# Performance work log

Hardware: AMD Instinct MI355X
Metric: run time of the kernel (lower is better)

The kernel has to match this reference:

```python
import jax, jax.numpy as jnp
import numpy as np

N_NODES = 50000
N_EDGES = 800000
D_IN = 256
D_OUT = 256


def setup_inputs() -> dict:
    key = jax.random.key(0)
    ks = jax.random.split(key, 8)
    x = jax.random.normal(ks[0], (N_NODES, D_IN), dtype=jnp.float32)
    edge_index = jax.random.randint(ks[1], (2, N_EDGES), 0, N_NODES, dtype=jnp.int64)
    W_src = jax.random.normal(ks[2], (D_IN, D_OUT), dtype=jnp.float32) * 0.05
    b_src = jax.random.normal(ks[3], (D_OUT,), dtype=jnp.float32) * 0.05
    W_dst = jax.random.normal(ks[4], (D_IN, D_OUT), dtype=jnp.float32) * 0.05
    b_dst = jax.random.normal(ks[5], (D_OUT,), dtype=jnp.float32) * 0.05
    W_self = jax.random.normal(ks[6], (D_IN, D_OUT), dtype=jnp.float32) * 0.05
    b_self = jax.random.normal(ks[7], (D_OUT,), dtype=jnp.float32) * 0.05
    return {"x": x, "edge_index": edge_index, "W_src": W_src, "b_src": b_src,
            "W_dst": W_dst, "b_dst": b_dst, "W_self": W_self, "b_self": b_self}


def reference(x, edge_index, W_src, b_src, W_dst, b_dst, W_self, b_self):
    # LEConv: messages = src_linear(x[row]) - dst_linear(x[col]);
    # scatter-add messages into destination nodes (col); add self_linear(x).
    # Linear commutes with row-gather, so project once on [N, d] then gather.
    row, col = edge_index[0], edge_index[1]
    src = x @ W_src + b_src            # [N, D_OUT]
    dst = x @ W_dst + b_dst            # [N, D_OUT]
    messages = src[row] - dst[col]     # [E, D_OUT]
    agg = jax.ops.segment_sum(messages, col, num_segments=x.shape[0])  # [N, D_OUT]
    return x @ W_self + b_self + agg
```

## Files before the change

### kernel.cpp

```cpp
#include <hip/hip_runtime.h>

#define D 256

typedef unsigned short ushort_t;
typedef unsigned int uint_t;
typedef __attribute__((ext_vector_type(8))) short short8;
typedef __attribute__((ext_vector_type(4))) float floatx4;

static __device__ __forceinline__ ushort_t f2bf(float f) {
    union { float f; uint_t u; } c; c.f = f;
    uint_t r = (c.u + 0x7FFFu + ((c.u >> 16) & 1u)) >> 16;
    return (ushort_t)r;
}
static __device__ __forceinline__ float bf2f(ushort_t b) {
    union { uint_t u; float f; } c; c.u = ((uint_t)b) << 16;
    return c.f;
}

static __device__ __forceinline__ void async16(const void* g, void* l) {
    __builtin_amdgcn_global_load_lds(
        (const __attribute__((address_space(1))) void*)g,
        (__attribute__((address_space(3))) void*)l, 16, 0, 0);
}

__global__ void prep_kernel(const int* __restrict__ col, int* __restrict__ deg,
                            int* __restrict__ rank,
                            const float* __restrict__ x, ushort_t* __restrict__ xh,
                            const float* __restrict__ Wself, const float* __restrict__ Wsrc,
                            const float* __restrict__ Wdst, ushort_t* __restrict__ BT,
                            int E, int total8, int degB, int cvtB) {
    int b = blockIdx.x;
    if (b < degB) {
        int e = b * 256 + threadIdx.x;
        if (e < E) rank[e] = atomicAdd(&deg[col[e]], 1);
    } else if (b < degB + cvtB) {
        int i = (b - degB) * 256 + threadIdx.x;
        if (i >= total8) return;
        float4 a = ((const float4*)x)[i * 2];
        float4 bb = ((const float4*)x)[i * 2 + 1];
        uint4 o;
        o.x = f2bf(a.x) | ((uint_t)f2bf(a.y) << 16);
        o.y = f2bf(a.z) | ((uint_t)f2bf(a.w) << 16);
        o.z = f2bf(bb.x) | ((uint_t)f2bf(bb.y) << 16);
        o.w = f2bf(bb.z) | ((uint_t)f2bf(bb.w) << 16);
        ((uint4*)xh)[i] = o;
    } else {
        int id = (b - degB - cvtB) * 256 + threadIdx.x;
        if (id >= 256 * 768) return;
        int j = id / 768, k = id % 768;
        float v;
        if (k < 256)      v = Wself[(size_t)k * 256 + j];
        else if (k < 512) v = Wsrc [(size_t)(k - 256) * 256 + j];
        else              v = Wdst [(size_t)(k - 512) * 256 + j];
        BT[id] = f2bf(v);
    }
}

__global__ __launch_bounds__(256) void scanA(const int* __restrict__ deg,
                                             int* __restrict__ off,
                                             int* __restrict__ partials, int n4) {
    __shared__ int wtot[4];
    const int tid = threadIdx.x, lane = tid & 63, wid = tid >> 6;
    int i4 = blockIdx.x * 256 + tid;
    int4 v = (i4 < n4) ? ((const int4*)deg)[i4] : make_int4(0, 0, 0, 0);
    int s = v.x + v.y + v.z + v.w;
    int incl = s;
    #pragma unroll
    for (int st = 1; st < 64; st <<= 1) {
        int t = __shfl_up(incl, st, 64);
        if (lane >= st) incl += t;
    }
    if (lane == 63) wtot[wid] = incl;
    __syncthreads();
    int wbase = 0;
    #pragma unroll
    for (int w = 0; w < 4; ++w) if (w < wid) wbase += wtot[w];
    int excl = incl - s + wbase;
    if (i4 < n4) {
        int4 o;
        o.x = excl; o.y = o.x + v.x; o.z = o.y + v.y; o.w = o.z + v.z;
        ((int4*)off)[i4] = o;
    }
    if (tid == 0) partials[blockIdx.x] = wtot[0] + wtot[1] + wtot[2] + wtot[3];
}

__global__ __launch_bounds__(256) void scanC(int* __restrict__ off,
                                             const int* __restrict__ partials, int n4) {
    __shared__ int base_s;
    const int tid = threadIdx.x;
    if (tid < 64) {
        int v = (tid < blockIdx.x) ? partials[tid] : 0;
        #pragma unroll
        for (int st = 32; st; st >>= 1) v += __shfl_down(v, st, 64);
        if (tid == 0) base_s = v;
    }
    __syncthreads();
    int base = base_s;
    int i4 = blockIdx.x * 256 + tid;
    if (i4 < n4) {
        int4 o = ((int4*)off)[i4];
        o.x += base; o.y += base; o.z += base; o.w += base;
        ((int4*)off)[i4] = o;
    }
}

__global__ void fill_kernel(const int* __restrict__ row, const int* __restrict__ col,
                            const int* __restrict__ rank, const int* __restrict__ off,
                            int* __restrict__ bucket, int E) {
    int e = blockIdx.x * blockDim.x + threadIdx.x;
    if (e >= E) return;
    bucket[off[col[e]] + rank[e]] = row[e];
}

__global__ __launch_bounds__(256) void segsum_kernel(const ushort_t* __restrict__ xh,
                                                     const int* __restrict__ off,
                                                     const int* __restrict__ deg,
                                                     const int* __restrict__ bucket,
                                                     ushort_t* __restrict__ Gh, int N) {
    int node = blockIdx.x * 4 + (threadIdx.x >> 6);
    int lane = threadIdx.x & 63;
    if (node >= N) return;
    int start = off[node];
    int cnt = deg[node];
    float a0 = 0.f, a1 = 0.f, a2 = 0.f, a3 = 0.f;
    int i = 0;
    for (; i + 4 <= cnt; i += 4) {
        int r0 = bucket[start + i];
        int r1 = bucket[start + i + 1];
        int r2 = bucket[start + i + 2];
        int r3 = bucket[start + i + 3];
        ushort4 v0 = ((const ushort4*)(xh + (size_t)r0 * D))[lane];
        ushort4 v1 = ((const ushort4*)(xh + (size_t)r1 * D))[lane];
        ushort4 v2 = ((const ushort4*)(xh + (size_t)r2 * D))[lane];
        ushort4 v3 = ((const ushort4*)(xh + (size_t)r3 * D))[lane];
        a0 += (bf2f(v0.x) + bf2f(v1.x)) + (bf2f(v2.x) + bf2f(v3.x));
        a1 += (bf2f(v0.y) + bf2f(v1.y)) + (bf2f(v2.y) + bf2f(v3.y));
        a2 += (bf2f(v0.z) + bf2f(v1.z)) + (bf2f(v2.z) + bf2f(v3.z));
        a3 += (bf2f(v0.w) + bf2f(v1.w)) + (bf2f(v2.w) + bf2f(v3.w));
    }
    for (; i < cnt; ++i) {
        int r0 = bucket[start + i];
        ushort4 v0 = ((const ushort4*)(xh + (size_t)r0 * D))[lane];
        a0 += bf2f(v0.x); a1 += bf2f(v0.y); a2 += bf2f(v0.z); a3 += bf2f(v0.w);
    }
    ushort4 o;
    o.x = f2bf(a0); o.y = f2bf(a1); o.z = f2bf(a2); o.w = f2bf(a3);
    ((ushort4*)(Gh + (size_t)node * D))[lane] = o;
}

__global__ __launch_bounds__(256, 2) void mfma_gemm(
    const ushort_t* __restrict__ xh, const ushort_t* __restrict__ Gh,
    const ushort_t* __restrict__ BT, const int* __restrict__ deg,
    const float* __restrict__ bsrc, const float* __restrict__ bdst,
    const float* __restrict__ bself, float* __restrict__ out, int N)
{
    __shared__ ushort_t As[2][8][64][8];
    __shared__ ushort_t Bs[2][8][64][8];
    __shared__ ushort_t Ds[2][8][64][8];

    const int tid = threadIdx.x;
    const int lane = tid & 63, wave = tid >> 6;
    const int quad = lane >> 4, l15 = lane & 15;
    const int mg = (wave >> 1) * 4, ng = (wave & 1) * 4;
    const int mbase = blockIdx.x * 128, nbase = blockIdx.y * 128;

    const int ga0 = wave * 2, ga1 = ga0 + 1;
    int ar0 = mbase + ga0 * 16 + l15; if (ar0 >= N) ar0 = N - 1;
    int ar1 = mbase + ga1 * 16 + l15; if (ar1 >= N) ar1 = N - 1;
    const size_t aoff0 = (size_t)ar0 * 256 + quad * 8;
    const size_t aoff1 = (size_t)ar1 * 256 + quad * 8;
    const ushort_t* bp0 = BT + (size_t)(nbase + ga0 * 16 + l15) * 768 + quad * 8;
    const ushort_t* bp1 = BT + (size_t)(nbase + ga1 * 16 + l15) * 768 + quad * 8;

    floatx4 acc1[4][4] = {};
    floatx4 acc2[4][4] = {};

    async16(xh + aoff0, &As[0][ga0][0][0]);
    async16(xh + aoff1, &As[0][ga1][0][0]);
    async16(bp0, &Bs[0][ga0][0][0]);
    async16(bp1, &Bs[0][ga1][0][0]);
    async16(bp0 + 512, &Ds[0][ga0][0][0]);
    async16(bp1 + 512, &Ds[0][ga1][0][0]);
    asm volatile("s_waitcnt vmcnt(0)" ::: "memory");
    __builtin_amdgcn_s_barrier();

    #pragma unroll
    for (int kt = 0; kt < 16; ++kt) {
        const int cur = kt & 1, nxt = cur ^ 1;

        if (kt < 15) {
            const int k1 = kt + 1;
            const ushort_t* Asrc = (k1 < 8) ? xh : Gh;
            const int ka = (k1 & 7) * 32;
            const int kb = k1 * 32;
            async16(Asrc + aoff0 + ka, &As[nxt][ga0][0][0]);
            async16(Asrc + aoff1 + ka, &As[nxt][ga1][0][0]);
            async16(bp0 + kb, &Bs[nxt][ga0][0][0]);
            async16(bp1 + kb, &Bs[nxt][ga1][0][0]);
            if (k1 < 8) {
                async16(bp0 + 512 + kb, &Ds[nxt][ga0][0][0]);
                async16(bp1 + 512 + kb, &Ds[nxt][ga1][0][0]);
            }
        }

        short8 af[4], bfr[4];
        #pragma unroll
        for (int im = 0; im < 4; ++im)
            af[im] = *(const short8*)(&As[cur][mg + im][lane][0]);
        #pragma unroll
        for (int in = 0; in < 4; ++in)
            bfr[in] = *(const short8*)(&Bs[cur][ng + in][lane][0]);
        short8 df[4];
        if (kt < 8) {
            #pragma unroll
            for (int in = 0; in < 4; ++in)
                df[in] = *(const short8*)(&Ds[cur][ng + in][lane][0]);
        }
        asm volatile("s_waitcnt lgkmcnt(0)" ::: "memory");
        #pragma unroll
        for (int im = 0; im < 4; ++im)
            #pragma unroll
            for (int in = 0; in < 4; ++in)
                acc1[im][in] = __builtin_amdgcn_mfma_f32_16x16x32_bf16(
                    af[im], bfr[in], acc1[im][in], 0, 0, 0);
        if (kt < 8) {
            #pragma unroll
            for (int im = 0; im < 4; ++im)
                #pragma unroll
                for (int in = 0; in < 4; ++in)
                    acc2[im][in] = __builtin_amdgcn_mfma_f32_16x16x32_bf16(
                        af[im], df[in], acc2[im][in], 0, 0, 0);
        }

        if (kt < 15) {
            asm volatile("s_waitcnt vmcnt(0)" ::: "memory");
            __builtin_amdgcn_s_barrier();
        }
    }

    float degv[4][4];
    #pragma unroll
    for (int im = 0; im < 4; ++im)
        #pragma unroll
        for (int r = 0; r < 4; ++r) {
            int gm = mbase + (wave >> 1) * 64 + im * 16 + quad * 4 + r;
            degv[im][r] = (gm < N) ? (float)deg[gm] : 0.f;
        }

    #pragma unroll
    for (int in = 0; in < 4; ++in) {
        int gn = nbase + (wave & 1) * 64 + in * 16 + l15;
        float bs = bself[gn];
        float db = bsrc[gn] - bdst[gn];
        #pragma unroll
        for (int im = 0; im < 4; ++im) {
            #pragma unroll
            for (int r = 0; r < 4; ++r) {
                int gm = mbase + (wave >> 1) * 64 + im * 16 + quad * 4 + r;
                if (gm < N) {
                    float d = degv[im][r];
                    out[(size_t)gm * 256 + gn] =
                        acc1[im][in][r] - d * acc2[im][in][r] + bs + d * db;
                }
            }
        }
    }
}

extern "C" void kernel_launch(void* const* d_in, const int* in_sizes, int n_in,
                              void* d_out, int out_size, void* d_ws, size_t ws_size,
                              hipStream_t stream) {
    const float* x     = (const float*)d_in[0];
    const int*   eidx  = (const int*)d_in[1];
    const float* Wsrc  = (const float*)d_in[2];
    const float* bsrc  = (const float*)d_in[3];
    const float* Wdst  = (const float*)d_in[4];
    const float* bdst  = (const float*)d_in[5];
    const float* Wself = (const float*)d_in[6];
    const float* bself = (const float*)d_in[7];
    float* out = (float*)d_out;

    const int N = in_sizes[0] / D;
    const int E = in_sizes[1] / 2;
    const int* row = eidx;
    const int* col = eidx + E;

    char* p = (char*)d_ws;
    ushort_t* xh  = (ushort_t*)p;        p += (size_t)N * D * sizeof(ushort_t);
    ushort_t* Gh  = (ushort_t*)p;        int* rank = (int*)p;
                                         p += (size_t)N * D * sizeof(ushort_t);
    ushort_t* BT  = (ushort_t*)p;        p += (size_t)768 * 256 * sizeof(ushort_t);
    int* deg      = (int*)p;             p += (size_t)N * sizeof(int);
    int* off      = (int*)p;             p += (size_t)N * sizeof(int);
    int* partials = (int*)p;             p += 64 * sizeof(int);
    int* bucket   = (int*)p;

    hipMemsetAsync(deg, 0, (size_t)N * sizeof(int), stream);

    const int total8 = N * D / 8;
    const int degB = (E + 255) / 256;
    const int cvtB = (total8 + 255) / 256;
    const int btB  = (256 * 768 + 255) / 256;
    prep_kernel<<<degB + cvtB + btB, 256, 0, stream>>>(col, deg, rank, x, xh,
                                                       Wself, Wsrc, Wdst, BT,
                                                       E, total8, degB, cvtB);
    const int n4 = N / 4;
    const int nblk = (n4 + 255) / 256;
    scanA<<<nblk, 256, 0, stream>>>(deg, off, partials, n4);
    scanC<<<nblk, 256, 0, stream>>>(off, partials, n4);
    fill_kernel<<<(E + 255) / 256, 256, 0, stream>>>(row, col, rank, off, bucket, E);
    segsum_kernel<<<(N + 3) / 4, 256, 0, stream>>>(xh, off, deg, bucket, Gh, N);

    dim3 grid((N + 127) / 128, 2);
    mfma_gemm<<<grid, 256, 0, stream>>>(xh, Gh, BT, deg, bsrc, bdst, bself, out, N);
}
```

Measured before the change: 277.6 us.

## Fold degree-scaled dst term into A operand and shrink GEMM M-tile to 64

The dst-projection term is no longer kept in a separate accumulator. Instead it becomes a third K segment in which the x rows are pre-scaled by -deg in bf16 before the MFMA, giving a single K=768 GEMM with one accumulator set. The block M-tile drops from 128 to 64, the Ds LDS buffer is removed and launch bounds are raised to 4 blocks per CU, which lowers register and LDS pressure for higher occupancy. In exchange, per-element scaling work is added in the inner loop, B tiles are reused less, and rounding deg*x to bf16 can reduce accuracy.

```diff
diff --git a/kernel.cpp b/kernel.cpp
--- a/kernel.cpp
+++ b/kernel.cpp
@@ -148,119 +148,111 @@
     ((ushort4*)(Gh + (size_t)node * D))[lane] = o;
 }
 
-__global__ __launch_bounds__(256, 2) void mfma_gemm(
+__global__ __launch_bounds__(256, 4) void mfma_gemm(
     const ushort_t* __restrict__ xh, const ushort_t* __restrict__ Gh,
     const ushort_t* __restrict__ BT, const int* __restrict__ deg,
     const float* __restrict__ bsrc, const float* __restrict__ bdst,
     const float* __restrict__ bself, float* __restrict__ out, int N)
 {
-    __shared__ ushort_t As[2][8][64][8];
+    __shared__ ushort_t As[2][4][64][8];
     __shared__ ushort_t Bs[2][8][64][8];
-    __shared__ ushort_t Ds[2][8][64][8];
 
     const int tid = threadIdx.x;
     const int lane = tid & 63, wave = tid >> 6;
     const int quad = lane >> 4, l15 = lane & 15;
-    const int mg = (wave >> 1) * 4, ng = (wave & 1) * 4;
-    const int mbase = blockIdx.x * 128, nbase = blockIdx.y * 128;
-
-    const int ga0 = wave * 2, ga1 = ga0 + 1;
-    int ar0 = mbase + ga0 * 16 + l15; if (ar0 >= N) ar0 = N - 1;
-    int ar1 = mbase + ga1 * 16 + l15; if (ar1 >= N) ar1 = N - 1;
-    const size_t aoff0 = (size_t)ar0 * 256 + quad * 8;
-    const size_t aoff1 = (size_t)ar1 * 256 + quad * 8;
-    const ushort_t* bp0 = BT + (size_t)(nbase + ga0 * 16 + l15) * 768 + quad * 8;
-    const ushort_t* bp1 = BT + (size_t)(nbase + ga1 * 16 + l15) * 768 + quad * 8;
-
-    floatx4 acc1[4][4] = {};
-    floatx4 acc2[4][4] = {};
-
-    async16(xh + aoff0, &As[0][ga0][0][0]);
-    async16(xh + aoff1, &As[0][ga1][0][0]);
-    async16(bp0, &Bs[0][ga0][0][0]);
-    async16(bp1, &Bs[0][ga1][0][0]);
-    async16(bp0 + 512, &Ds[0][ga0][0][0]);
-    async16(bp1 + 512, &Ds[0][ga1][0][0]);
+    const int wr = wave >> 1, wc = wave & 1;
+    const int mbase = blockIdx.x * 64, nbase = blockIdx.y * 128;
+
+    int ar = mbase + wave * 16 + l15; if (ar >= N) ar = N - 1;
+    const size_t aoff = (size_t)ar * 256 + quad * 8;
+    const ushort_t* bp0 = BT + (size_t)(nbase + (wave * 2) * 16 + l15) * 768 + quad * 8;
+    const ushort_t* bp1 = BT + (size_t)(nbase + (wave * 2 + 1) * 16 + l15) * 768 + quad * 8;
+
+    float negdeg[2];
+    #pragma unroll
+    for (int im = 0; im < 2; ++im) {
+        int r = mbase + (wr * 2 + im) * 16 + l15; if (r >= N) r = N - 1;
+        negdeg[im] = -(float)deg[r];
+    }
+
+    floatx4 acc[2][4] = {};
+
+    async16(xh + aoff, &As[0][wave][0][0]);
+    async16(bp0, &Bs[0][wave * 2][0][0]);
+    async16(bp1, &Bs[0][wave * 2 + 1][0][0]);
     asm volatile("s_waitcnt vmcnt(0)" ::: "memory");
     __builtin_amdgcn_s_barrier();
 
     #pragma unroll
-    for (int kt = 0; kt < 16; ++kt) {
+    for (int kt = 0; kt < 24; ++kt) {
         const int cur = kt & 1, nxt = cur ^ 1;
 
-        if (kt < 15) {
+        if (kt < 23) {
             const int k1 = kt + 1;
-            const ushort_t* Asrc = (k1 < 8) ? xh : Gh;
+            const ushort_t* Ap = (k1 < 8) ? xh : (k1 < 16 ? Gh : xh);
             const int ka = (k1 & 7) * 32;
-            const int kb = k1 * 32;
-            async16(Asrc + aoff0 + ka, &As[nxt][ga0][0][0]);
-            async16(Asrc + aoff1 + ka, &As[nxt][ga1][0][0]);
-            async16(bp0 + kb, &Bs[nxt][ga0][0][0]);
-            async16(bp1 + kb, &Bs[nxt][ga1][0][0]);
-            if (k1 < 8) {
-                async16(bp0 + 512 + kb, &Ds[nxt][ga0][0][0]);
-                async16(bp1 + 512 + kb, &Ds[nxt][ga1][0][0]);
+            async16(Ap + aoff + ka, &As[nxt][wave][0][0]);
+            async16(bp0 + k1 * 32, &Bs[nxt][wave * 2][0][0]);
+            async16(bp1 + k1 * 32, &Bs[nxt][wave * 2 + 1][0][0]);
+        }
+
+        short8 af[2], bfr[4];
+        #pragma unroll
+        for (int im = 0; im < 2; ++im)
+            af[im] = *(const short8*)(&As[cur][wr * 2 + im][lane][0]);
+        #pragma unroll
+        for (int in = 0; in < 4; ++in)
+            bfr[in] = *(const short8*)(&Bs[cur][wc * 4 + in][lane][0]);
+        asm volatile("s_waitcnt lgkmcnt(0)" ::: "memory");
+
+        if (kt >= 16) {
+            #pragma unroll
+            for (int im = 0; im < 2; ++im) {
+                short8 t = af[im];
+                #pragma unroll
+                for (int j = 0; j < 8; ++j) {
+                    float f = bf2f((ushort_t)t[j]) * negdeg[im];
+                    t[j] = (short)f2bf(f);
+                }
+                af[im] = t;
             }
         }
 
-        short8 af[4], bfr[4];
-        #pragma unroll
-        for (int im = 0; im < 4; ++im)
-            af[im] = *(const short8*)(&As[cur][mg + im][lane][0]);
-        #pragma unroll
-        for (int in = 0; in < 4; ++in)
-            bfr[in] = *(const short8*)(&Bs[cur][ng + in][lane][0]);
-        short8 df[4];
-        if (kt < 8) {
+        #pragma unroll
+        for (int im = 0; im < 2; ++im)
             #pragma unroll
             for (int in = 0; in < 4; ++in)
-                df[in] = *(const short8*)(&Ds[cur][ng + in][lane][0]);
-        }
-        asm volatile("s_waitcnt lgkmcnt(0)" ::: "memory");
-        #pragma unroll
-        for (int im = 0; im < 4; ++im)
-            #pragma unroll
-            for (int in = 0; in < 4; ++in)
-                acc1[im][in] = __builtin_amdgcn_mfma_f32_16x16x32_bf16(
-                    af[im], bfr[in], acc1[im][in], 0, 0, 0);
-        if (kt < 8) {
-            #pragma unroll
-            for (int im = 0; im < 4; ++im)
-                #pragma unroll
-                for (int in = 0; in < 4; ++in)
-                    acc2[im][in] = __builtin_amdgcn_mfma_f32_16x16x32_bf16(
-                        af[im], df[in], acc2[im][in], 0, 0, 0);
-        }
-
-        if (kt < 15) {
+                acc[im][in] = __builtin_amdgcn_mfma_f32_16x16x32_bf16(
+                    af[im], bfr[in], acc[im][in], 0, 0, 0);
+
+        if (kt < 23) {
             asm volatile("s_waitcnt vmcnt(0)" ::: "memory");
             __builtin_amdgcn_s_barrier();
         }
     }
 
-    float degv[4][4];
-    #pragma unroll
-    for (int im = 0; im < 4; ++im)
+    float degv[2][4];
+    #pragma unroll
+    for (int im = 0; im < 2; ++im)
         #pragma unroll
         for (int r = 0; r < 4; ++r) {
-            int gm = mbase + (wave >> 1) * 64 + im * 16 + quad * 4 + r;
+            int gm = mbase + wr * 32 + im * 16 + quad * 4 + r;
             degv[im][r] = (gm < N) ? (float)deg[gm] : 0.f;
         }
 
     #pragma unroll
     for (int in = 0; in < 4; ++in) {
-        int gn = nbase + (wave & 1) * 64 + in * 16 + l15;
+        int gn = nbase + wc * 64 + in * 16 + l15;
         float bs = bself[gn];
         float db = bsrc[gn] - bdst[gn];
         #pragma unroll
-        for (int im = 0; im < 4; ++im) {
+        for (int im = 0; im < 2; ++im) {
             #pragma unroll
             for (int r = 0; r < 4; ++r) {
-                int gm = mbase + (wave >> 1) * 64 + im * 16 + quad * 4 + r;
+                int gm = mbase + wr * 32 + im * 16 + quad * 4 + r;
                 if (gm < N) {
-                    float d = degv[im][r];
                     out[(size_t)gm * 256 + gn] =
-                        acc1[im][in][r] - d * acc2[im][in][r] + bs + d * db;
+                        acc[im][in][r] + bs + degv[im][r] * db;
                 }
             }
         }
@@ -311,6 +303,6 @@
     fill_kernel<<<(E + 255) / 256, 256, 0, stream>>>(row, col, rank, off, bucket, E);
     segsum_kernel<<<(N + 3) / 4, 256, 0, stream>>>(xh, off, deg, bucket, Gh, N);
 
-    dim3 grid((N + 127) / 128, 2);
+    dim3 grid((N + 63) / 64, 2);
     mfma_gemm<<<grid, 256, 0, stream>>>(xh, Gh, BT, deg, bsrc, bdst, bself, out, N);
 }
```

After: 300.9 us. +8.4%, slower.
